# Optimization experiments

Measured on AMD Instinct MI355X. Metric: run time of the kernel, lower is better.

Reference implementation:

```python
import jax, jax.numpy as jnp
import numpy as np
import math

H, D, DEG = 8, 64, 2
GATE_BIAS = 6.906768

def _rope(x, sin, cos):
    # GPT-J style interleaved rotary: even lanes = x1*cos - x2*sin, odd = x2*cos + x1*sin
    x1, x2 = x[..., ::2], x[..., 1::2]
    s = sin[None, :, None, :]
    c = cos[None, :, None, :]
    even = x1 * c - x2 * s
    odd = x2 * c + x1 * s
    return jnp.stack([even, odd], axis=-1).reshape(x.shape)

def _forward(x, w_attn, w_proj):
    B, T, C = x.shape
    h, d, deg = H, D, DEG
    hd = h * d
    scale = 1.0 / math.sqrt(d)
    qkvg = x @ w_attn                                   # (B,T,3hd+h)
    q = qkvg[..., :hd].reshape(B, T, h, d)
    k = qkvg[..., hd:2 * hd].reshape(B, T, h, d)
    v = qkvg[..., 2 * hd:3 * hd].reshape(B, T, h, d)
    log_g = jax.nn.log_sigmoid(GATE_BIAS + qkvg[..., 3 * hd:].astype(jnp.float32))  # (B,T,h)
    # sinusoidal RoPE with frequency 2*pi / T**(2i/d), as in get_sinusoidal_embeddings
    pos = jnp.arange(T, dtype=jnp.float32)
    div = 2.0 * math.pi / (float(T) ** (jnp.arange(0, d, 2, dtype=jnp.float32) / d))
    ang = pos[:, None] * div[None, :]                   # (T, d//2)
    sin, cos = jnp.sin(ang), jnp.cos(ang)
    q = _rope(q, sin, cos)
    k = _rope(k, sin, cos)
    # gated symmetric-power attention: quadratic reference of chunked power_full
    # score_ts = (scale * q_t . k_s)^deg * exp(L_t - L_s), causal, row-normalized
    L = jnp.cumsum(log_g, axis=1).transpose(0, 2, 1)    # (B,h,T) cumulative log-gates
    qk = jnp.einsum('bthd,bshd->bhts', q, k) * scale    # (B,h,T,T)
    log_gate = L[:, :, :, None] - L[:, :, None, :]      # L_t - L_s
    causal = jnp.tril(jnp.ones((T, T), dtype=bool))
    scores = jnp.where(causal, (qk ** deg) * jnp.exp(log_gate), 0.0)
    denom = jnp.maximum(scores.sum(-1, keepdims=True), 1e-6)
    y = jnp.einsum('bhts,bshd->bthd', scores / denom, v)  # (B,T,h,d)
    return y.reshape(B, T, hd) @ w_proj

def setup_inputs() -> dict:
    key = jax.random.key(0)
    k1, k2, k3 = jax.random.split(key, 3)
    B, T, C = 2, 2048, 512
    x = jax.random.normal(k1, (B, T, C), dtype=jnp.float32)
    w_attn = jax.random.normal(k2, (C, 3 * H * D + H), dtype=jnp.float32) * 0.02
    w_proj = jax.random.normal(k3, (H * D, C), dtype=jnp.float32) * 0.02
    return {"x": x, "w_attn": w_attn, "w_proj": w_proj}

def reference(x, w_attn, w_proj):
    return _forward(x, w_attn, w_proj)
```

## Files before the change

### kernel.cpp

```cpp
#include <hip/hip_runtime.h>
#include <math.h>

constexpr int B_ = 2, T_ = 2048, C_ = 512, H_ = 8, D_ = 64;
constexpr int QKVG_ = 3 * H_ * D_ + H_;
constexpr float GATE_BIAS_ = 6.906768f;
constexpr int N1_ = 1536;
constexpr int SC_ = 8;
constexpr int NBLK_ = 1280;
constexpr int MC_ = 4096 * 512;
constexpr int BHT_ = B_ * H_ * T_;

typedef __attribute__((ext_vector_type(8))) short short8;
typedef __attribute__((ext_vector_type(4))) float f32x4;

__device__ __forceinline__ unsigned short f2b(float f) {
    unsigned int u = __float_as_uint(f);
    unsigned int r = (u + 0x7fffu + ((u >> 16) & 1u)) >> 16;
    return (unsigned short)r;
}
__device__ __forceinline__ short8 pack8(float4 a, float4 b) {
    short8 r;
    r[0] = (short)f2b(a.x); r[1] = (short)f2b(a.y);
    r[2] = (short)f2b(a.z); r[3] = (short)f2b(a.w);
    r[4] = (short)f2b(b.x); r[5] = (short)f2b(b.y);
    r[6] = (short)f2b(b.z); r[7] = (short)f2b(b.w);
    return r;
}

__device__ __forceinline__ void gl2lds16(const unsigned short* g, void* lds_base) {
    __builtin_amdgcn_global_load_lds(
        (const __attribute__((address_space(1))) unsigned int*)g,
        (__attribute__((address_space(3))) unsigned int*)lds_base, 16, 0, 0);
}

__device__ __forceinline__ void packT_body(
    const float* __restrict__ W, unsigned short* __restrict__ Bt,
    int K, int N, int ldW, int nt, int kt, int tid, float (*Ws)[65])
{
    {
        const int r = tid >> 2;
        const int c0 = (tid & 3) * 16;
#pragma unroll
        for (int j = 0; j < 16; ++j) {
            const int n = nt + c0 + j;
            Ws[r][c0 + j] = (n < N) ? W[(size_t)(kt + r) * ldW + n] : 0.f;
        }
    }
    __syncthreads();
    {
        const int d = tid >> 2;
        const int cc = tid & 3;
        const int kc = cc * 16;
        short8 o0, o1;
#pragma unroll
        for (int j = 0; j < 8; ++j) o0[j] = (short)f2b(Ws[kc + j][d]);
#pragma unroll
        for (int j = 0; j < 8; ++j) o1[j] = (short)f2b(Ws[kc + 8 + j][d]);
        const int row = nt + d;
        unsigned short* op = Bt + (size_t)row * K + kt;
        *(short8*)(op + ((2 * cc) ^ (row & 7)) * 8)     = o0;
        *(short8*)(op + ((2 * cc + 1) ^ (row & 7)) * 8) = o1;
    }
}

__global__ __launch_bounds__(256) void pack_inputs(
    const float* __restrict__ x, const float* __restrict__ w_attn,
    const float* __restrict__ w_proj, unsigned short* __restrict__ xb,
    unsigned short* __restrict__ Bt1, unsigned short* __restrict__ Bt2,
    float2* __restrict__ sincos, float* __restrict__ g)
{
    __shared__ float SM[64 * 65];
    float (*Ws)[65] = (float(*)[65])SM;
    const int bid = blockIdx.x;
    const int tid = threadIdx.x;
    if (bid < 1024) {
        const int i = bid * 256 + tid;
        float4 f0 = *(const float4*)(x + (size_t)i * 8);
        float4 f1 = *(const float4*)(x + (size_t)i * 8 + 4);
        const int row = i >> 6;
        const int ic = i & 63;
        const int swc = (ic & ~7) | ((ic & 7) ^ (row & 7));
        *(short8*)(xb + (size_t)row * 512 + swc * 8) = pack8(f0, f1);
    } else if (bid < 1216) {
        const int q = bid - 1024;
        packT_body(w_attn, Bt1, C_, N1_, QKVG_, (q % 24) * 64, (q / 24) * 64, tid, Ws);
    } else if (bid < 1280) {
        const int q = bid - 1216;
        packT_body(w_proj, Bt2, H_ * D_, C_, C_, (q & 7) * 64, (q >> 3) * 64, tid, Ws);
    } else if (bid < 1288) {
        const int t = (bid - 1280) * 256 + tid;
        float2* op = sincos + (size_t)t * 32;
#pragma unroll
        for (int i = 0; i < 32; ++i) {
            const float div = 6.2831853071795864f * exp2f((float)i * (-11.0f / 32.0f));
            const float ang = (float)t * div;
            op[i] = make_float2(cosf(ang), sinf(ang));
        }
    } else {
        const int q = bid - 1288;
        float* LDSw = SM;
        {
            const int k = tid * 2;
#pragma unroll
            for (int kk = 0; kk < 2; ++kk) {
                const float* wp = w_attn + (size_t)(k + kk) * QKVG_ + 1536;
                float4 wa = *(const float4*)wp;
                float4 wb = *(const float4*)(wp + 4);
                float* dst = LDSw + (k + kk) * 8;
                *(float4*)dst = wa;
                *(float4*)(dst + 4) = wb;
            }
        }
        __syncthreads();
        const int m = q * 32 + (tid >> 3);
        const int h = tid & 7;
        const float* xrow = x + (size_t)m * C_;
        float s = 0.f;
#pragma unroll 4
        for (int k0 = 0; k0 < 512; k0 += 4) {
            float4 xv = *(const float4*)(xrow + k0);
            s += xv.x * LDSw[(k0 + 0) * 8 + h] + xv.y * LDSw[(k0 + 1) * 8 + h]
               + xv.z * LDSw[(k0 + 2) * 8 + h] + xv.w * LDSw[(k0 + 3) * 8 + h];
        }
        const int b = m >> 11, t = m & 2047;
        g[(size_t)(b * 8 + h) * T_ + t] = s;
    }
}

__global__ __launch_bounds__(256) void gate_cumsum(
    const float* __restrict__ g, float* __restrict__ Lg)
{
    __shared__ float wsum[4];
    const int bh = blockIdx.x;
    const int tid = threadIdx.x;
    const int lane = tid & 63, wv = tid >> 6;

    const float* gp = g + (size_t)bh * T_ + tid * 8;
    float v[8];
    float s = 0.f;
#pragma unroll
    for (int j = 0; j < 8; ++j) {
        const float z = gp[j] + GATE_BIAS_;
        const float lg = (z > 0.f) ? -log1pf(expf(-z)) : (z - log1pf(expf(z)));
        s += lg;
        v[j] = s;
    }
    float ssum = s;
#pragma unroll
    for (int off = 1; off < 64; off <<= 1) {
        float n = __shfl_up(ssum, off, 64);
        if (lane >= off) ssum += n;
    }
    if (lane == 63) wsum[wv] = ssum;
    __syncthreads();
    float base = ssum - s;
#pragma unroll
    for (int w = 0; w < 3; ++w)
        base += (w < wv) ? wsum[w] : 0.f;

    float* op = Lg + (size_t)bh * T_ + tid * 8;
#pragma unroll
    for (int j = 0; j < 8; ++j) op[j] = v[j] + base;
}

__global__ __launch_bounds__(256) void gemm_fused(
    const unsigned short* __restrict__ A, const unsigned short* __restrict__ Bt,
    const float* __restrict__ Lg, const float2* __restrict__ sincos,
    unsigned short* __restrict__ Qsb, unsigned short* __restrict__ Ksb,
    unsigned short* __restrict__ Vtb)
{
    __shared__ __align__(16) char smem[33280];
    char* AsB = smem;
    char* BsB = smem + 16384;
    float (*epi)[65] = (float(*)[65])smem;

    const int tid = threadIdx.x;
    const int wave = tid >> 6, lane = tid & 63;
    const int l15 = lane & 15, lhi = lane >> 4;
    const int wr = wave >> 1, wc = wave & 1;
    const int bm = blockIdx.y * 128, bn = blockIdx.x * 128;

    f32x4 acc[4][4];
#pragma unroll
    for (int i = 0; i < 4; ++i)
#pragma unroll
        for (int j = 0; j < 4; ++j) acc[i][j] = (f32x4){0.f, 0.f, 0.f, 0.f};

    const unsigned short* Arow = A + (size_t)bm * C_;
    const unsigned short* Brow = Bt + (size_t)bn * C_;
    const int sw = (l15 & 7) << 4;
    const int srow = tid >> 3;
    const int schunk = tid & 7;

    for (int k0 = 0; k0 < C_; k0 += 64) {
        __syncthreads();
#pragma unroll
        for (int p = 0; p < 4; ++p) {
            const int row = p * 32 + srow;
            const size_t goff = (size_t)row * C_ + k0 + schunk * 8;
            gl2lds16(Arow + goff, AsB + p * 4096 + wave * 1024);
            gl2lds16(Brow + goff, BsB + p * 4096 + wave * 1024);
        }
        __syncthreads();

        short8 af[4][2];
#pragma unroll
        for (int mi = 0; mi < 4; ++mi) {
            const int row = wr * 64 + mi * 16 + l15;
#pragma unroll
            for (int kk = 0; kk < 2; ++kk)
                af[mi][kk] = *(const short8*)(AsB + row * 128 + ((kk * 64 + lhi * 16) ^ sw));
        }
#pragma unroll
        for (int ni = 0; ni < 4; ++ni) {
            const int row = wc * 64 + ni * 16 + l15;
            short8 bf0 = *(const short8*)(BsB + row * 128 + ((lhi * 16) ^ sw));
            short8 bf1 = *(const short8*)(BsB + row * 128 + ((64 + lhi * 16) ^ sw));
#pragma unroll
            for (int mi = 0; mi < 4; ++mi) {
                acc[mi][ni] = __builtin_amdgcn_mfma_f32_16x16x32_bf16(af[mi][0], bf0, acc[mi][ni], 0, 0, 0);
                acc[mi][ni] = __builtin_amdgcn_mfma_f32_16x16x32_bf16(af[mi][1], bf1, acc[mi][ni], 0, 0, 0);
            }
        }
    }

    const int rid = bn >> 9;
    const int b = bm >> 11;
    const int tloc0 = bm & 2047;

#pragma unroll
    for (int hc = 0; hc < 2; ++hc) {
        __syncthreads();
        if (wc == hc) {
#pragma unroll
            for (int mi = 0; mi < 4; ++mi)
#pragma unroll
                for (int ni = 0; ni < 4; ++ni)
#pragma unroll
                    for (int r = 0; r < 4; ++r)
                        epi[wr * 64 + mi * 16 + lhi * 4 + r][ni * 16 + l15] = acc[mi][ni][r];
        }
        __syncthreads();
        const int h = ((bn & 511) >> 6) + hc;
        const int bh = b * 8 + h;
        if (rid < 2) {
            const int row = tid >> 1;
            const int c0 = (tid & 1) * 32;
            const int t = tloc0 + row;
            const float Lt = Lg[(size_t)bh * T_ + t];
            const float scl = (rid == 0) ? (__expf(0.5f * Lt) * 0.125f)
                                         : __expf(-0.5f * Lt);
            float vb[32];
#pragma unroll
            for (int j = 0; j < 32; ++j) vb[j] = epi[row][c0 + j];
            const float2* sct = sincos + (size_t)t * 32 + (c0 >> 1);
#pragma unroll
            for (int p = 0; p < 16; ++p) {
                const float2 cssn = sct[p];
                const float x1 = vb[2 * p], x2 = vb[2 * p + 1];
                vb[2 * p]     = (x1 * cssn.x - x2 * cssn.y) * scl;
                vb[2 * p + 1] = (x2 * cssn.x + x1 * cssn.y) * scl;
            }
            unsigned short* op = ((rid == 0) ? Qsb : Ksb) + ((size_t)bh * T_ + t) * 64;
#pragma unroll
            for (int j = 0; j < 4; ++j) {
                short8 o = pack8(*(float4*)&vb[j * 8], *(float4*)&vb[j * 8 + 4]);
                const int chunk = (c0 >> 3) + j;
                const int pos = (rid == 0) ? chunk : (chunk ^ (t & 7));
                *(short8*)(op + pos * 8) = o;
            }
        } else {
            const int d = tid >> 2;
            const int tq = tid & 3;
            unsigned short* op = Vtb + ((size_t)(bh * 64 + d)) * T_;
#pragma unroll
            for (int j = 0; j < 4; ++j) {
                const int tl = tq * 32 + j * 8;
                short8 o;
#pragma unroll
                for (int e = 0; e < 8; ++e)
                    o[e] = (short)f2b(epi[tl + e][d]);
                const int chunkidx = (tloc0 + tl) >> 3;
                const int pos = (chunkidx & ~7) | ((chunkidx & 7) ^ (d & 7));
                *(short8*)(op + pos * 8) = o;
            }
        }
    }
}

__global__ __launch_bounds__(256) void gemm_bf16(
    const unsigned short* __restrict__ A, const unsigned short* __restrict__ Bt,
    float* __restrict__ C, int M, int N, int K)
{
    __shared__ __align__(16) char AsB[128 * 128];
    __shared__ __align__(16) char BsB[128 * 128];

    const int tid = threadIdx.x;
    const int wave = tid >> 6, lane = tid & 63;
    const int l15 = lane & 15, lhi = lane >> 4;
    const int wr = wave >> 1, wc = wave & 1;
    const int bm = blockIdx.y * 128, bn = blockIdx.x * 128;

    f32x4 acc[4][4];
#pragma unroll
    for (int i = 0; i < 4; ++i)
#pragma unroll
        for (int j = 0; j < 4; ++j) acc[i][j] = (f32x4){0.f, 0.f, 0.f, 0.f};

    const unsigned short* Arow = A + (size_t)bm * K;
    const unsigned short* Brow = Bt + (size_t)bn * K;
    const int sw = (l15 & 7) << 4;
    const int srow = tid >> 3;
    const int schunk = tid & 7;

    for (int k0 = 0; k0 < K; k0 += 64) {
        __syncthreads();
#pragma unroll
        for (int p = 0; p < 4; ++p) {
            const int row = p * 32 + srow;
            const size_t goff = (size_t)row * K + k0 + schunk * 8;
            gl2lds16(Arow + goff, AsB + p * 4096 + wave * 1024);
            gl2lds16(Brow + goff, BsB + p * 4096 + wave * 1024);
        }
        __syncthreads();

        short8 af[4][2];
#pragma unroll
        for (int mi = 0; mi < 4; ++mi) {
            const int row = wr * 64 + mi * 16 + l15;
#pragma unroll
            for (int kk = 0; kk < 2; ++kk)
                af[mi][kk] = *(const short8*)(AsB + row * 128 + ((kk * 64 + lhi * 16) ^ sw));
        }
#pragma unroll
        for (int ni = 0; ni < 4; ++ni) {
            const int row = wc * 64 + ni * 16 + l15;
            short8 bf0 = *(const short8*)(BsB + row * 128 + ((lhi * 16) ^ sw));
            short8 bf1 = *(const short8*)(BsB + row * 128 + ((64 + lhi * 16) ^ sw));
#pragma unroll
            for (int mi = 0; mi < 4; ++mi) {
                acc[mi][ni] = __builtin_amdgcn_mfma_f32_16x16x32_bf16(af[mi][0], bf0, acc[mi][ni], 0, 0, 0);
                acc[mi][ni] = __builtin_amdgcn_mfma_f32_16x16x32_bf16(af[mi][1], bf1, acc[mi][ni], 0, 0, 0);
            }
        }
    }

#pragma unroll
    for (int mi = 0; mi < 4; ++mi) {
        const int gm = bm + wr * 64 + mi * 16 + lhi * 4;
#pragma unroll
        for (int r = 0; r < 4; ++r) {
            float* crow = C + (size_t)(gm + r) * N;
#pragma unroll
            for (int ni = 0; ni < 4; ++ni) {
                const int gn = bn + wc * 64 + ni * 16 + l15;
                if (gn < N) crow[gn] = acc[mi][ni][r];
            }
        }
    }
}

__global__ __launch_bounds__(256) void attn_mfma(
    const unsigned short* __restrict__ Qsb, const unsigned short* __restrict__ Ksb,
    const unsigned short* __restrict__ Vtb,
    float* __restrict__ Y0, float* __restrict__ Yp, float* __restrict__ Dpart)
{
    __shared__ __align__(16) char smem[24576];
    char* KsB = smem;
    char* VtB = smem + 8192;
    char* PsB = smem + 16384;

    const int wg = blockIdx.x;
    const int xcd = wg & 7;
    const int slot = wg >> 3;
    const int bh = (slot < 80) ? xcd : 8 + xcd;
    const int rem = (slot < 80) ? slot : slot - 80;
    const int rr = 79 - rem;
    int bt, sc;
    if (rr < 8)       { bt = rr; sc = 0; }
    else if (rr < 24) { const int q = rr - 8;  bt = 8 + (q >> 1);  sc = q & 1; }
    else if (rr < 48) { const int q = rr - 24; bt = 16 + q / 3;    sc = q % 3; }
    else              { const int q = rr - 48; bt = 24 + (q >> 2); sc = q & 3; }
    const int st0 = sc * SC_;
    const int st1 = min(st0 + SC_ - 1, bt);

    const int tid = threadIdx.x;
    const int wave = tid >> 6;
    const int lane = tid & 63;
    const int l15 = lane & 15;
    const int lhi = lane >> 4;
    const int b = bh >> 3, h = bh & 7;
    const int t0 = bt * 64;

    const int qrow = t0 + wave * 16 + l15;
    const unsigned short* qpp = Qsb + ((size_t)bh * T_ + qrow) * 64 + lhi * 8;
    short8 qf[2];
    qf[0] = *(const short8*)(qpp);
    qf[1] = *(const short8*)(qpp + 32);

    f32x4 accY[4];
#pragma unroll
    for (int n = 0; n < 4; ++n) accY[n] = (f32x4){0.f, 0.f, 0.f, 0.f};
    float den[4] = {0.f, 0.f, 0.f, 0.f};

    const int kchunk = lhi * 16;
    const int rsw = (l15 & 7) << 4;
    const int srow = tid >> 3;
    const int schunk = tid & 7;

    for (int st = st0; st <= st1; ++st) {
        __syncthreads();
#pragma unroll
        for (int p = 0; p < 2; ++p) {
            const int row = p * 32 + srow;
            gl2lds16(Ksb + ((size_t)bh * T_ + st * 64 + row) * 64 + schunk * 8,
                     KsB + p * 4096 + wave * 1024);
            gl2lds16(Vtb + ((size_t)bh * 64 + row) * T_ + st * 64 + schunk * 8,
                     VtB + p * 4096 + wave * 1024);
        }
        __syncthreads();

        f32x4 accS[4];
#pragma unroll
        for (int n = 0; n < 4; ++n) accS[n] = (f32x4){0.f, 0.f, 0.f, 0.f};
#pragma unroll
        for (int n = 0; n < 4; ++n) {
#pragma unroll
            for (int kk = 0; kk < 2; ++kk) {
                short8 bf = *(const short8*)(KsB + (n * 16 + l15) * 128 + ((kk * 64 + kchunk) ^ rsw));
                accS[n] = __builtin_amdgcn_mfma_f32_16x16x32_bf16(qf[kk], bf, accS[n], 0, 0, 0);
            }
        }

        const bool last = (st == bt);
        char* PsW = PsB + wave * 2048;
#pragma unroll
        for (int n = 0; n < 4; ++n) {
#pragma unroll
            for (int r = 0; r < 4; ++r) {
                const float a = accS[n][r];
                float p = a * a;
                if (last)
                    p = ((n * 16 + l15) <= wave * 16 + lhi * 4 + r) ? p : 0.f;
                den[r] += p;
                const int prow = lhi * 4 + r;
                *(unsigned short*)(PsW + prow * 128 + ((2 * (n * 16 + l15)) ^ ((prow & 7) << 4))) = f2b(p);
            }
        }

        short8 pa[2];
#pragma unroll
        for (int kk = 0; kk < 2; ++kk)
            pa[kk] = *(const short8*)(PsW + l15 * 128 + ((kk * 64 + kchunk) ^ rsw));
#pragma unroll
        for (int n = 0; n < 4; ++n) {
#pragma unroll
            for (int kk = 0; kk < 2; ++kk) {
                short8 vb = *(const short8*)(VtB + (n * 16 + l15) * 128 + ((kk * 64 + kchunk) ^ rsw));
                accY[n] = __builtin_amdgcn_mfma_f32_16x16x32_bf16(pa[kk], vb, accY[n], 0, 0, 0);
            }
        }
    }

#pragma unroll
    for (int r = 0; r < 4; ++r) {
        den[r] += __shfl_xor(den[r], 1, 64);
        den[r] += __shfl_xor(den[r], 2, 64);
        den[r] += __shfl_xor(den[r], 4, 64);
        den[r] += __shfl_xor(den[r], 8, 64);
    }

    float* Ybase = (sc == 0) ? Y0 : (Yp + (size_t)(sc - 1) * MC_);
    float* Dbase = Dpart + (size_t)sc * BHT_;
#pragma unroll
    for (int r = 0; r < 4; ++r) {
        const int t = t0 + wave * 16 + lhi * 4 + r;
        if (l15 == 0)
            Dbase[(size_t)bh * T_ + t] = den[r];
        float* yo = Ybase + (size_t)(b * T_ + t) * (H_ * D_) + h * 64 + l15;
#pragma unroll
        for (int n = 0; n < 4; ++n)
            yo[n * 16] = accY[n][r];
    }
}

__global__ __launch_bounds__(256) void normalize_kernel(
    const float* __restrict__ Y0, const float* __restrict__ Yp,
    const float* __restrict__ Dpart, unsigned short* __restrict__ ybb)
{
    const int gid = blockIdx.x * 256 + threadIdx.x;
    const size_t base = (size_t)gid * 8;
    const int row = (int)(base >> 9);
    const int col = (int)(base & 511);
    const int b = row >> 11, t = row & 2047, h = col >> 6;
    const int bh = b * H_ + h;
    const int nsc = ((t >> 6) >> 3) + 1;

    float d = Dpart[(size_t)bh * T_ + t];
    float4 f0 = *(const float4*)(Y0 + base);
    float4 f1 = *(const float4*)(Y0 + base + 4);
    for (int s = 1; s < nsc; ++s) {
        d += Dpart[(size_t)s * BHT_ + (size_t)bh * T_ + t];
        const float* yp = Yp + (size_t)(s - 1) * MC_ + base;
        float4 g0 = *(const float4*)(yp);
        float4 g1 = *(const float4*)(yp + 4);
        f0.x += g0.x; f0.y += g0.y; f0.z += g0.z; f0.w += g0.w;
        f1.x += g1.x; f1.y += g1.y; f1.z += g1.z; f1.w += g1.w;
    }
    const float inv = 1.0f / fmaxf(d, 1e-6f);
    f0.x *= inv; f0.y *= inv; f0.z *= inv; f0.w *= inv;
    f1.x *= inv; f1.y *= inv; f1.z *= inv; f1.w *= inv;

    const int ic = col >> 3;
    const int swc = (ic & ~7) | ((ic & 7) ^ (row & 7));
    *(short8*)(ybb + (size_t)row * 512 + swc * 8) = pack8(f0, f1);
}

extern "C" void kernel_launch(void* const* d_in, const int* in_sizes, int n_in,
                              void* d_out, int out_size, void* d_ws, size_t ws_size,
                              hipStream_t stream)
{
    const float* x      = (const float*)d_in[0];
    const float* w_attn = (const float*)d_in[1];
    const float* w_proj = (const float*)d_in[2];
    float* out = (float*)d_out;

    char* p = (char*)d_ws;
    float2* sincos = (float2*)p;               p += (size_t)T_ * 32 * 8;
    float* g       = (float*)p;                p += (size_t)BHT_ * 4;
    float* Lg      = (float*)p;                p += (size_t)BHT_ * 4;
    float* Dpart   = (float*)p;                p += (size_t)4 * BHT_ * 4;
    unsigned short* xb  = (unsigned short*)p;  p += (size_t)MC_ * 2;
    unsigned short* Bt1 = (unsigned short*)p;  p += (size_t)N1_ * C_ * 2;
    unsigned short* Bt2 = (unsigned short*)p;  p += (size_t)C_ * C_ * 2;
    unsigned short* Qsb = (unsigned short*)p;  p += (size_t)BHT_ * 64 * 2;
    unsigned short* Ksb = (unsigned short*)p;  p += (size_t)BHT_ * 64 * 2;
    unsigned short* Vtb = (unsigned short*)p;  p += (size_t)BHT_ * 64 * 2;
    float* Yp      = (float*)p;                p += (size_t)3 * MC_ * 4;
    unsigned short* ybb = (unsigned short*)p;

    const int M = B_ * T_;

    pack_inputs<<<1416, 256, 0, stream>>>(x, w_attn, w_proj, xb, Bt1, Bt2, sincos, g);

    gate_cumsum<<<B_ * H_, 256, 0, stream>>>(g, Lg);

    gemm_fused<<<dim3(N1_ / 128, M / 128), 256, 0, stream>>>(
        xb, Bt1, Lg, sincos, Qsb, Ksb, Vtb);

    attn_mfma<<<NBLK_, 256, 0, stream>>>(Qsb, Ksb, Vtb, out, Yp, Dpart);

    normalize_kernel<<<(MC_ / 8) / 256, 256, 0, stream>>>(out, Yp, Dpart, ybb);

    gemm_bf16<<<dim3(C_ / 128, M / 128), 256, 0, stream>>>(
        ybb, Bt2, out, M, C_, H_ * D_);
}
```

Before: 84.24 us.

## Double-buffer LDS tiles in GEMM and attention kernels to overlap loads with MFMA

The fused QKV GEMM, the plain bf16 GEMM and the attention kernel now keep two LDS buffers. The first tile is loaded before the loop, and each iteration issues the next tile's global-to-LDS copy before computing on the current one. This drops one barrier per iteration and lets memory traffic overlap the MFMA work. In exchange, LDS use roughly doubles: 64 KB per block for the GEMMs and 40 KB for attention. That can cut the number of resident blocks per CU and the latency hiding that came from occupancy.

```diff
diff --git a/kernel.cpp b/kernel.cpp
--- a/kernel.cpp
+++ b/kernel.cpp
@@ -169,9 +169,7 @@
     unsigned short* __restrict__ Qsb, unsigned short* __restrict__ Ksb,
     unsigned short* __restrict__ Vtb)
 {
-    __shared__ __align__(16) char smem[33280];
-    char* AsB = smem;
-    char* BsB = smem + 16384;
+    __shared__ __align__(16) char smem[65536];
     float (*epi)[65] = (float(*)[65])smem;
 
     const int tid = threadIdx.x;
@@ -192,16 +190,29 @@
     const int srow = tid >> 3;
     const int schunk = tid & 7;
 
-    for (int k0 = 0; k0 < C_; k0 += 64) {
+#pragma unroll
+    for (int p = 0; p < 4; ++p) {
+        const int row = p * 32 + srow;
+        const size_t goff = (size_t)row * C_ + schunk * 8;
+        gl2lds16(Arow + goff, smem + p * 4096 + wave * 1024);
+        gl2lds16(Brow + goff, smem + 16384 + p * 4096 + wave * 1024);
+    }
+
+    for (int ks = 0; ks < 8; ++ks) {
         __syncthreads();
-#pragma unroll
-        for (int p = 0; p < 4; ++p) {
-            const int row = p * 32 + srow;
-            const size_t goff = (size_t)row * C_ + k0 + schunk * 8;
-            gl2lds16(Arow + goff, AsB + p * 4096 + wave * 1024);
-            gl2lds16(Brow + goff, BsB + p * 4096 + wave * 1024);
-        }
-        __syncthreads();
+        if (ks < 7) {
+            char* dst = smem + ((ks + 1) & 1) * 32768;
+            const int k1 = (ks + 1) * 64;
+#pragma unroll
+            for (int p = 0; p < 4; ++p) {
+                const int row = p * 32 + srow;
+                const size_t goff = (size_t)row * C_ + k1 + schunk * 8;
+                gl2lds16(Arow + goff, dst + p * 4096 + wave * 1024);
+                gl2lds16(Brow + goff, dst + 16384 + p * 4096 + wave * 1024);
+            }
+        }
+        const char* AsB = smem + (ks & 1) * 32768;
+        const char* BsB = AsB + 16384;
 
         short8 af[4][2];
 #pragma unroll
@@ -292,8 +303,7 @@
     const unsigned short* __restrict__ A, const unsigned short* __restrict__ Bt,
     float* __restrict__ C, int M, int N, int K)
 {
-    __shared__ __align__(16) char AsB[128 * 128];
-    __shared__ __align__(16) char BsB[128 * 128];
+    __shared__ __align__(16) char smem[65536];
 
     const int tid = threadIdx.x;
     const int wave = tid >> 6, lane = tid & 63;
@@ -312,17 +322,31 @@
     const int sw = (l15 & 7) << 4;
     const int srow = tid >> 3;
     const int schunk = tid & 7;
-
-    for (int k0 = 0; k0 < K; k0 += 64) {
+    const int nks = K >> 6;
+
+#pragma unroll
+    for (int p = 0; p < 4; ++p) {
+        const int row = p * 32 + srow;
+        const size_t goff = (size_t)row * K + schunk * 8;
+        gl2lds16(Arow + goff, smem + p * 4096 + wave * 1024);
+        gl2lds16(Brow + goff, smem + 16384 + p * 4096 + wave * 1024);
+    }
+
+    for (int ks = 0; ks < nks; ++ks) {
         __syncthreads();
-#pragma unroll
-        for (int p = 0; p < 4; ++p) {
-            const int row = p * 32 + srow;
-            const size_t goff = (size_t)row * K + k0 + schunk * 8;
-            gl2lds16(Arow + goff, AsB + p * 4096 + wave * 1024);
-            gl2lds16(Brow + goff, BsB + p * 4096 + wave * 1024);
-        }
-        __syncthreads();
+        if (ks + 1 < nks) {
+            char* dst = smem + ((ks + 1) & 1) * 32768;
+            const int k1 = (ks + 1) * 64;
+#pragma unroll
+            for (int p = 0; p < 4; ++p) {
+                const int row = p * 32 + srow;
+                const size_t goff = (size_t)row * K + k1 + schunk * 8;
+                gl2lds16(Arow + goff, dst + p * 4096 + wave * 1024);
+                gl2lds16(Brow + goff, dst + 16384 + p * 4096 + wave * 1024);
+            }
+        }
+        const char* AsB = smem + (ks & 1) * 32768;
+        const char* BsB = AsB + 16384;
 
         short8 af[4][2];
 #pragma unroll
@@ -365,10 +389,8 @@
     const unsigned short* __restrict__ Vtb,
     float* __restrict__ Y0, float* __restrict__ Yp, float* __restrict__ Dpart)
 {
-    __shared__ __align__(16) char smem[24576];
-    char* KsB = smem;
-    char* VtB = smem + 8192;
-    char* PsB = smem + 16384;
+    __shared__ __align__(16) char smem[40960];
+    char* PsB = smem + 32768;
 
     const int wg = blockIdx.x;
     const int xcd = wg & 7;
@@ -408,17 +430,31 @@
     const int srow = tid >> 3;
     const int schunk = tid & 7;
 
+#pragma unroll
+    for (int p = 0; p < 2; ++p) {
+        const int row = p * 32 + srow;
+        gl2lds16(Ksb + ((size_t)bh * T_ + st0 * 64 + row) * 64 + schunk * 8,
+                 smem + p * 4096 + wave * 1024);
+        gl2lds16(Vtb + ((size_t)bh * 64 + row) * T_ + st0 * 64 + schunk * 8,
+                 smem + 8192 + p * 4096 + wave * 1024);
+    }
+
     for (int st = st0; st <= st1; ++st) {
         __syncthreads();
-#pragma unroll
-        for (int p = 0; p < 2; ++p) {
-            const int row = p * 32 + srow;
-            gl2lds16(Ksb + ((size_t)bh * T_ + st * 64 + row) * 64 + schunk * 8,
-                     KsB + p * 4096 + wave * 1024);
-            gl2lds16(Vtb + ((size_t)bh * 64 + row) * T_ + st * 64 + schunk * 8,
-                     VtB + p * 4096 + wave * 1024);
-        }
-        __syncthreads();
+        if (st < st1) {
+            char* dst = smem + (((st - st0) + 1) & 1) * 16384;
+            const int s1 = (st + 1) * 64;
+#pragma unroll
+            for (int p = 0; p < 2; ++p) {
+                const int row = p * 32 + srow;
+                gl2lds16(Ksb + ((size_t)bh * T_ + s1 + row) * 64 + schunk * 8,
+                         dst + p * 4096 + wave * 1024);
+                gl2lds16(Vtb + ((size_t)bh * 64 + row) * T_ + s1 + schunk * 8,
+                         dst + 8192 + p * 4096 + wave * 1024);
+            }
+        }
+        const char* KsB = smem + ((st - st0) & 1) * 16384;
+        const char* VtB = KsB + 8192;
 
         f32x4 accS[4];
 #pragma unroll
```

After: 79.81 us. 1.06x faster.
